# Optimization experiments

Hardware: AMD Instinct MI355X
Metric: run time of the kernel (lower is better)

The kernel has to match this reference:

```python
import jax, jax.numpy as jnp
import numpy as np

N, G, D, F, A = 50000, 128, 32, 64, 8
N_ITERS, N_BLAYERS = 3, 3
EPS = 1e-5
HIN = D + F + 2 * F * A  # 1120: input to transform_out


def setup_inputs() -> dict:
    key = jax.random.key(0)
    ks = jax.random.split(key, 10)
    p = lambda k, shape: jax.random.normal(k, shape, jnp.float32) * 0.05
    return {
        "x": jax.random.normal(ks[0], (N, 3), jnp.float32),
        "batch": jnp.sort(jax.random.randint(ks[1], (N,), 0, G)),
        # input_network: Linear(3,D) + LayerNorm(D) + Tanh
        "Wi": p(ks[2], (3, D)), "bi": jnp.zeros((D,), jnp.float32),
        "lni_w": jnp.ones((D,), jnp.float32), "lni_b": jnp.zeros((D,), jnp.float32),
        # 3 BipartiteLayers (weights shared across graph iterations, stacked over layer idx)
        "W_in": p(ks[3], (N_BLAYERS, D, F)), "b_in": jnp.zeros((N_BLAYERS, F), jnp.float32),
        "W_sc": p(ks[4], (N_BLAYERS, F, A)), "b_sc": jnp.zeros((N_BLAYERS, A), jnp.float32),
        "W_out": p(ks[5], (N_BLAYERS, HIN, D)), "b_out": jnp.zeros((N_BLAYERS, D), jnp.float32),
        # PyG graph-mode LayerNorm after each BipartiteLayer
        "gln_w": jnp.ones((N_BLAYERS, D), jnp.float32), "gln_b": jnp.zeros((N_BLAYERS, D), jnp.float32),
        "Wp": p(ks[6], (3, D, D)), "bp": jnp.zeros((3, D), jnp.float32),
        "lnp_w": jnp.ones((3, D), jnp.float32), "lnp_b": jnp.zeros((3, D), jnp.float32),
        "Wpo": p(ks[7], (D, 1)), "bpo": jnp.zeros((1,), jnp.float32),
    }


def _ln(x, w, b):  # nn.LayerNorm over last dim
    m = x.mean(-1, keepdims=True)
    v = ((x - m) ** 2).mean(-1, keepdims=True)
    return (x - m) / jnp.sqrt(v + EPS) * w + b


def _graph_ln(x, w, b):  # PyG gnn.norm.LayerNorm, mode='graph', batch=None
    xc = x - x.mean()
    std = jnp.sqrt((xc * xc).mean())
    return xc / (std + EPS) * w + b


def _bipartite(x, batch, counts, Win, bin_, Wsc, bsc, Wout, bout):
    xp = x @ Win + bin_                                  # (N,F)
    attn = jnp.exp(-jnp.abs(xp @ Wsc + bsc))             # (N,A) 'potential' activation
    w = attn[:, :, None] * xp[:, None, :]                # (N,A,F) == einsum('nf,na->naf')
    sums = jax.ops.segment_sum(w, batch, num_segments=G)  # (G,A,F)
    cnt = counts[:, None, None]
    mean_p = sums / jnp.maximum(cnt, 1.0)
    max_p = jax.ops.segment_max(w, batch, num_segments=G)
    max_p = jnp.where(cnt > 0, max_p, 0.0)               # torch_scatter zero-fill for empty
    agg = jnp.concatenate([mean_p, max_p], axis=-1).reshape(G, 2 * F * A)  # (G,A,2F)->(G,2FA)
    H = jnp.concatenate([x, xp, agg[batch]], axis=-1)    # (N, HIN)
    return jnp.tanh(H @ Wout + bout)                     # Tanh hidden activation


def reference(x, batch, Wi, bi, lni_w, lni_b, W_in, b_in, W_sc, b_sc, W_out, b_out,
              gln_w, gln_b, Wp, bp, lnp_w, lnp_b, Wpo, bpo):
    counts = jax.ops.segment_sum(jnp.ones((x.shape[0],), x.dtype), batch, num_segments=G)
    h = jnp.tanh(_ln(x @ Wi + bi, lni_w, lni_b))
    for _ in range(N_ITERS):
        for j in range(N_BLAYERS):
            h = _bipartite(h, batch, counts, W_in[j], b_in[j], W_sc[j], b_sc[j], W_out[j], b_out[j])
            h = _graph_ln(h, gln_w[j], gln_b[j])
    s = jax.ops.segment_sum(h, batch, num_segments=G) / jnp.maximum(counts, 1.0)[:, None]  # scatter_mean
    for j in range(3):
        s = jnp.tanh(_ln(s @ Wp[j] + bp[j], lnp_w[j], lnp_b[j]))
    return (s @ Wpo + bpo).squeeze(-1)  # (G,)
```

## Files before the change

kernel.cpp:

```cpp
#include <hip/hip_runtime.h>
#include <math.h>

#define NPTS 50000
#define NG   128
#define DD   32
#define FF   64
#define AA   8
#define HINC 1120
#define EPSV 1e-5f
#define CH   64

__device__ __forceinline__ float tanh_fast(float x) {
    float e = __expf(-2.f * fabsf(x));
    float r = __fdividef(1.f - e, 1.f + e);
    return copysignf(r, x);
}

__global__ __launch_bounds__(256) void k_setup(const int* __restrict__ batch,
                                               const float* __restrict__ W_in,
                                               const float* __restrict__ b_in,
                                               const float* __restrict__ W_out,
                                               const float* __restrict__ b_out,
                                               int* __restrict__ offs,
                                               float* __restrict__ stats,
                                               float* __restrict__ Weff,
                                               float* __restrict__ beff) {
    int t = threadIdx.x, bid = blockIdx.x;
    if (bid == 0) {
        if (t <= NG) {
            int lo = 0, hi = NPTS;
            while (lo < hi) { int mid = (lo+hi)>>1; if (batch[mid] < t) lo = mid+1; else hi = mid; }
            offs[t] = lo;
        }
        if (t < 32) stats[t] = 0.f;
    } else {
        int j = bid - 1;
        const float* W0 = W_out + (size_t)j*HINC*DD;
        const float* W1 = W0 + DD*DD;
        const float* Wi = W_in + (size_t)j*DD*FF;
        for (int e = t; e < DD*DD; e += 256) {
            int i = e >> 5, d = e & 31;
            float s = W0[e];
            for (int f = 0; f < FF; f++) s += Wi[i*FF+f] * W1[f*DD+d];
            Weff[j*DD*DD + e] = s;
        }
        if (t < DD) {
            float s = b_out[j*DD + t];
            for (int f = 0; f < FF; f++) s += b_in[j*FF+f] * W1[f*DD+t];
            beff[j*DD + t] = s;
        }
    }
}

__global__ __launch_bounds__(512) void k_L(const float* __restrict__ x,
                                           const float* __restrict__ Wi,
                                           const float* __restrict__ bi,
                                           const float* __restrict__ lniw,
                                           const float* __restrict__ lnib,
                                           const float* __restrict__ inb,
                                           const float* __restrict__ stats,
                                           const float* __restrict__ gw,
                                           const float* __restrict__ gb,
                                           const float* __restrict__ Win,
                                           const float* __restrict__ bin,
                                           const float* __restrict__ Wsc,
                                           const float* __restrict__ bsc,
                                           const int* __restrict__ offs,
                                           const float* __restrict__ Wagg,
                                           const float* __restrict__ beff,
                                           const float* __restrict__ Weff,
                                           float* __restrict__ tbuf,
                                           float* __restrict__ statsO,
                                           int isL0) {
    int g = blockIdx.x;
    int gs = offs[g], cnt = offs[g+1] - gs;
    const int t = threadIdx.x;
    if (cnt <= 0) return;

    __shared__ float hs[CH][36];
    __shared__ float sxp[CH][68];
    __shared__ float sattn[CH][9];
    __shared__ float sWin[DD*FF];
    __shared__ float sScT[AA*FF];
    __shared__ float sW[DD][36];
    __shared__ float agg[2*FF*AA];
    __shared__ float red[16][DD];
    __shared__ float aggWs[DD];
    __shared__ float sbin[FF];
    __shared__ float shW[DD];
    __shared__ float rs1[8], rs2[8];

    ((float4*)sWin)[t] = ((const float4*)Win)[t];
    { int a = t >> 6, f = t & 63; sScT[t] = Wsc[f*AA + a]; }
    for (int k = t; k < DD*DD; k += 512) sW[k >> 5][k & 31] = Weff[k];

    float gm = 0.f, ginv = 1.f;
    if (!isL0) {
        const float invM = 1.f/((float)NPTS*DD);
        gm = stats[0]*invM;
        float var = stats[1]*invM - gm*gm;
        ginv = 1.f/(sqrtf(fmaxf(var, 0.f)) + EPSV);
    }
    __syncthreads();
    if (!isL0) {
        if (t < FF) {
            float b = bin[t];
            for (int k = 0; k < DD; k++) {
                float sk = ginv * gw[k];
                float sh = gb[k] - gm * sk;
                b += sh * sWin[k*FF + t];
            }
            sbin[t] = b;
        } else if (t < FF + DD) {
            int d = t - FF;
            float r = 0.f;
            for (int k = 0; k < DD; k++) {
                float sk = ginv * gw[k];
                float sh = gb[k] - gm * sk;
                r += sh * sW[k][d];
            }
            shW[d] = r;
        }
        __syncthreads();
        for (int e = t; e < DD*FF; e += 512) sWin[e] *= ginv * gw[e >> 6];
        for (int e = t; e < DD*DD; e += 512) sW[e >> 5][e & 31] *= ginv * gw[e >> 5];
        __syncthreads();
    } else {
        if (t < FF) sbin[t] = bin[t];
        else if (t < FF + DD) shW[t - FF] = 0.f;
        __syncthreads();
    }

    const int pt = t >> 3, q = t & 7;
    const int fo = q * 8;
    const int ca = t >> 6, cf = t & 63;
    const float bscv = bsc[q];
    const float4 bi0 = *(const float4*)&sbin[fo];
    const float4 bi1 = *(const float4*)&sbin[fo+4];
    float csum = 0.f, cmax = -INFINITY;

    if (isL0) {
        for (int base = gs; base < gs + cnt; base += CH) {
            int np = min(CH, gs + cnt - base);
            __syncthreads();
            {
                int pp = t >> 3, d4 = (t & 7)*4;
                if (pp < np) {
                    int n = base + pp;
                    float x0 = x[n*3], x1 = x[n*3+1], x2 = x[n*3+2];
                    float tv0 = x0*Wi[d4+0] + x1*Wi[DD+d4+0] + x2*Wi[2*DD+d4+0] + bi[d4+0];
                    float tv1 = x0*Wi[d4+1] + x1*Wi[DD+d4+1] + x2*Wi[2*DD+d4+1] + bi[d4+1];
                    float tv2 = x0*Wi[d4+2] + x1*Wi[DD+d4+2] + x2*Wi[2*DD+d4+2] + bi[d4+2];
                    float tv3 = x0*Wi[d4+3] + x1*Wi[DD+d4+3] + x2*Wi[2*DD+d4+3] + bi[d4+3];
                    float sm = (tv0+tv1) + (tv2+tv3);
                    sm += __shfl_xor(sm, 1); sm += __shfl_xor(sm, 2); sm += __shfl_xor(sm, 4);
                    float mm = sm * (1.f/DD);
                    float c0 = tv0-mm, c1 = tv1-mm, c2 = tv2-mm, c3 = tv3-mm;
                    float qq = (c0*c0 + c1*c1) + (c2*c2 + c3*c3);
                    qq += __shfl_xor(qq, 1); qq += __shfl_xor(qq, 2); qq += __shfl_xor(qq, 4);
                    float inv = 1.f/sqrtf(qq*(1.f/DD) + EPSV);
                    hs[pp][d4+0] = tanh_fast(c0*inv*lniw[d4+0] + lnib[d4+0]);
                    hs[pp][d4+1] = tanh_fast(c1*inv*lniw[d4+1] + lnib[d4+1]);
                    hs[pp][d4+2] = tanh_fast(c2*inv*lniw[d4+2] + lnib[d4+2]);
                    hs[pp][d4+3] = tanh_fast(c3*inv*lniw[d4+3] + lnib[d4+3]);
                }
            }
            __syncthreads();
            if (pt < np) {
                float xr[8] = {bi0.x,bi0.y,bi0.z,bi0.w,bi1.x,bi1.y,bi1.z,bi1.w};
                #pragma unroll
                for (int k = 0; k < DD; k++) {
                    float hv = hs[pt][k];
                    float4 wa = *(const float4*)&sWin[k*FF + fo];
                    float4 wb = *(const float4*)&sWin[k*FF + fo + 4];
                    xr[0] += hv*wa.x; xr[1] += hv*wa.y; xr[2] += hv*wa.z; xr[3] += hv*wa.w;
                    xr[4] += hv*wb.x; xr[5] += hv*wb.y; xr[6] += hv*wb.z; xr[7] += hv*wb.w;
                }
                float pa[8];
                #pragma unroll
                for (int a = 0; a < 8; a++) {
                    float4 wa = *(const float4*)&sScT[a*FF + fo];
                    float4 wb = *(const float4*)&sScT[a*FF + fo + 4];
                    pa[a] = xr[0]*wa.x + xr[1]*wa.y + xr[2]*wa.z + xr[3]*wa.w
                          + xr[4]*wb.x + xr[5]*wb.y + xr[6]*wb.z + xr[7]*wb.w;
                }
                #pragma unroll
                for (int msk = 1; msk < 8; msk <<= 1) {
                    #pragma unroll
                    for (int a = 0; a < 8; a++) pa[a] += __shfl_xor(pa[a], msk);
                }
                sattn[pt][q] = __expf(-fabsf(pa[q] + bscv));
                *(float4*)&sxp[pt][fo]   = make_float4(xr[0],xr[1],xr[2],xr[3]);
                *(float4*)&sxp[pt][fo+4] = make_float4(xr[4],xr[5],xr[6],xr[7]);
            }
            __syncthreads();
            for (int pp = 0; pp < np; pp++) {
                float w = sattn[pp][ca] * sxp[pp][cf];
                csum += w; cmax = fmaxf(cmax, w);
            }
        }
    } else {
        float4 cur[8], nxt[8];
        {
            int n0 = gs + min(pt, cnt-1);
            const float4* r4 = (const float4*)(inb + (size_t)n0*DD);
            #pragma unroll
            for (int j = 0; j < 8; j++) cur[j] = r4[j];
        }
        for (int base = gs; base < gs + cnt; base += CH) {
            int np = min(CH, gs + cnt - base);
            {
                int nb = base + CH;
                int nclamp = (nb < gs + cnt) ? min(nb + pt, gs + cnt - 1) : gs;
                const float4* r4 = (const float4*)(inb + (size_t)nclamp*DD);
                #pragma unroll
                for (int j = 0; j < 8; j++) nxt[j] = r4[j];
            }
            __syncthreads();
            if (pt < np) {
                float xr[8] = {bi0.x,bi0.y,bi0.z,bi0.w,bi1.x,bi1.y,bi1.z,bi1.w};
                #pragma unroll
                for (int k4 = 0; k4 < 8; k4++) {
                    float hv0 = cur[k4].x, hv1 = cur[k4].y, hv2 = cur[k4].z, hv3 = cur[k4].w;
                    int kb = k4*4;
                    float4 wa, wb;
                    wa = *(const float4*)&sWin[(kb+0)*FF + fo]; wb = *(const float4*)&sWin[(kb+0)*FF + fo + 4];
                    xr[0]+=hv0*wa.x; xr[1]+=hv0*wa.y; xr[2]+=hv0*wa.z; xr[3]+=hv0*wa.w;
                    xr[4]+=hv0*wb.x; xr[5]+=hv0*wb.y; xr[6]+=hv0*wb.z; xr[7]+=hv0*wb.w;
                    wa = *(const float4*)&sWin[(kb+1)*FF + fo]; wb = *(const float4*)&sWin[(kb+1)*FF + fo + 4];
                    xr[0]+=hv1*wa.x; xr[1]+=hv1*wa.y; xr[2]+=hv1*wa.z; xr[3]+=hv1*wa.w;
                    xr[4]+=hv1*wb.x; xr[5]+=hv1*wb.y; xr[6]+=hv1*wb.z; xr[7]+=hv1*wb.w;
                    wa = *(const float4*)&sWin[(kb+2)*FF + fo]; wb = *(const float4*)&sWin[(kb+2)*FF + fo + 4];
                    xr[0]+=hv2*wa.x; xr[1]+=hv2*wa.y; xr[2]+=hv2*wa.z; xr[3]+=hv2*wa.w;
                    xr[4]+=hv2*wb.x; xr[5]+=hv2*wb.y; xr[6]+=hv2*wb.z; xr[7]+=hv2*wb.w;
                    wa = *(const float4*)&sWin[(kb+3)*FF + fo]; wb = *(const float4*)&sWin[(kb+3)*FF + fo + 4];
                    xr[0]+=hv3*wa.x; xr[1]+=hv3*wa.y; xr[2]+=hv3*wa.z; xr[3]+=hv3*wa.w;
                    xr[4]+=hv3*wb.x; xr[5]+=hv3*wb.y; xr[6]+=hv3*wb.z; xr[7]+=hv3*wb.w;
                }
                float pa[8];
                #pragma unroll
                for (int a = 0; a < 8; a++) {
                    float4 wa = *(const float4*)&sScT[a*FF + fo];
                    float4 wb = *(const float4*)&sScT[a*FF + fo + 4];
                    pa[a] = xr[0]*wa.x + xr[1]*wa.y + xr[2]*wa.z + xr[3]*wa.w
                          + xr[4]*wb.x + xr[5]*wb.y + xr[6]*wb.z + xr[7]*wb.w;
                }
                #pragma unroll
                for (int msk = 1; msk < 8; msk <<= 1) {
                    #pragma unroll
                    for (int a = 0; a < 8; a++) pa[a] += __shfl_xor(pa[a], msk);
                }
                sattn[pt][q] = __expf(-fabsf(pa[q] + bscv));
                *(float4*)&sxp[pt][fo]   = make_float4(xr[0],xr[1],xr[2],xr[3]);
                *(float4*)&sxp[pt][fo+4] = make_float4(xr[4],xr[5],xr[6],xr[7]);
            }
            __syncthreads();
            for (int pp = 0; pp < np; pp++) {
                float w = sattn[pp][ca] * sxp[pp][cf];
                csum += w; cmax = fmaxf(cmax, w);
            }
            #pragma unroll
            for (int j = 0; j < 8; j++) cur[j] = nxt[j];
        }
    }

    agg[ca*2*FF + cf]      = csum / (float)cnt;
    agg[ca*2*FF + FF + cf] = cmax;
    __syncthreads();
    {
        int d = t & 31, grp = t >> 5;
        float acc = 0.f;
        #pragma unroll
        for (int k2 = 0; k2 < 64; k2++) {
            int k = grp*64 + k2;
            acc += agg[k] * Wagg[k*DD + d];
        }
        red[grp][d] = acc;
    }
    __syncthreads();
    if (t < DD) {
        float r = 0.f;
        #pragma unroll
        for (int qq = 0; qq < 16; qq++) r += red[qq][t];
        aggWs[t] = r + beff[t] + shW[t];
    }
    __syncthreads();

    float s1 = 0.f, s2a = 0.f;
    const int d4 = q * 4;
    if (isL0) {
        for (int base = gs; base < gs + cnt; base += CH) {
            int np = min(CH, gs + cnt - base);
            __syncthreads();
            {
                int pp = t >> 3;
                if (pp < np) {
                    int n = base + pp;
                    float x0 = x[n*3], x1 = x[n*3+1], x2 = x[n*3+2];
                    float tv0 = x0*Wi[d4+0] + x1*Wi[DD+d4+0] + x2*Wi[2*DD+d4+0] + bi[d4+0];
                    float tv1 = x0*Wi[d4+1] + x1*Wi[DD+d4+1] + x2*Wi[2*DD+d4+1] + bi[d4+1];
                    float tv2 = x0*Wi[d4+2] + x1*Wi[DD+d4+2] + x2*Wi[2*DD+d4+2] + bi[d4+2];
                    float tv3 = x0*Wi[d4+3] + x1*Wi[DD+d4+3] + x2*Wi[2*DD+d4+3] + bi[d4+3];
                    float sm = (tv0+tv1) + (tv2+tv3);
                    sm += __shfl_xor(sm, 1); sm += __shfl_xor(sm, 2); sm += __shfl_xor(sm, 4);
                    float mm = sm * (1.f/DD);
                    float c0 = tv0-mm, c1 = tv1-mm, c2 = tv2-mm, c3 = tv3-mm;
                    float qq = (c0*c0 + c1*c1) + (c2*c2 + c3*c3);
                    qq += __shfl_xor(qq, 1); qq += __shfl_xor(qq, 2); qq += __shfl_xor(qq, 4);
                    float inv = 1.f/sqrtf(qq*(1.f/DD) + EPSV);
                    hs[pp][d4+0] = tanh_fast(c0*inv*lniw[d4+0] + lnib[d4+0]);
                    hs[pp][d4+1] = tanh_fast(c1*inv*lniw[d4+1] + lnib[d4+1]);
                    hs[pp][d4+2] = tanh_fast(c2*inv*lniw[d4+2] + lnib[d4+2]);
                    hs[pp][d4+3] = tanh_fast(c3*inv*lniw[d4+3] + lnib[d4+3]);
                }
            }
            __syncthreads();
            {
                int pp = t >> 3;
                if (pp < np) {
                    int n = base + pp;
                    float4 a0 = *(const float4*)&aggWs[d4];
                    float acc0 = a0.x, acc1 = a0.y, acc2 = a0.z, acc3 = a0.w;
                    #pragma unroll
                    for (int k = 0; k < DD; k++) {
                        float hv = hs[pp][k];
                        float4 w = *(const float4*)&sW[k][d4];
                        acc0 += hv*w.x; acc1 += hv*w.y; acc2 += hv*w.z; acc3 += hv*w.w;
                    }
                    float4 o;
                    o.x = tanh_fast(acc0); o.y = tanh_fast(acc1);
                    o.z = tanh_fast(acc2); o.w = tanh_fast(acc3);
                    *(float4*)&tbuf[(size_t)n*DD + d4] = o;
                    s1  += (o.x + o.y) + (o.z + o.w);
                    s2a += (o.x*o.x + o.y*o.y) + (o.z*o.z + o.w*o.w);
                }
            }
        }
    } else {
        float4 rcur[8], rnxt[8];
        if (pt < cnt) {
            {
                const float4* r4 = (const float4*)(inb + (size_t)(gs + pt)*DD);
                #pragma unroll
                for (int j = 0; j < 8; j++) rcur[j] = r4[j];
            }
            float4 a0 = *(const float4*)&aggWs[d4];
            for (int n = gs + pt; n < gs + cnt; n += CH) {
                int nn = n + CH;
                int nclamp = (nn < gs + cnt) ? nn : n;
                {
                    const float4* r4 = (const float4*)(inb + (size_t)nclamp*DD);
                    #pragma unroll
                    for (int j = 0; j < 8; j++) rnxt[j] = r4[j];
                }
                float acc0 = a0.x, acc1 = a0.y, acc2 = a0.z, acc3 = a0.w;
                #pragma unroll
                for (int k4 = 0; k4 < 8; k4++) {
                    float hv0 = rcur[k4].x, hv1 = rcur[k4].y, hv2 = rcur[k4].z, hv3 = rcur[k4].w;
                    int kb = k4*4;
                    float4 w;
                    w = *(const float4*)&sW[kb+0][d4];
                    acc0 += hv0*w.x; acc1 += hv0*w.y; acc2 += hv0*w.z; acc3 += hv0*w.w;
                    w = *(const float4*)&sW[kb+1][d4];
                    acc0 += hv1*w.x; acc1 += hv1*w.y; acc2 += hv1*w.z; acc3 += hv1*w.w;
                    w = *(const float4*)&sW[kb+2][d4];
                    acc0 += hv2*w.x; acc1 += hv2*w.y; acc2 += hv2*w.z; acc3 += hv2*w.w;
                    w = *(const float4*)&sW[kb+3][d4];
                    acc0 += hv3*w.x; acc1 += hv3*w.y; acc2 += hv3*w.z; acc3 += hv3*w.w;
                }
                float4 o;
                o.x = tanh_fast(acc0); o.y = tanh_fast(acc1);
                o.z = tanh_fast(acc2); o.w = tanh_fast(acc3);
                *(float4*)&tbuf[(size_t)n*DD + d4] = o;
                s1  += (o.x + o.y) + (o.z + o.w);
                s2a += (o.x*o.x + o.y*o.y) + (o.z*o.z + o.w*o.w);
                #pragma unroll
                for (int j = 0; j < 8; j++) rcur[j] = rnxt[j];
            }
        }
    }
    #pragma unroll
    for (int o = 32; o > 0; o >>= 1) { s1 += __shfl_down(s1, o); s2a += __shfl_down(s2a, o); }
    int wid = t >> 6;
    __syncthreads();
    if ((t & 63) == 0) { rs1[wid] = s1; rs2[wid] = s2a; }
    __syncthreads();
    if (t == 0) {
        float a1 = 0.f, a2 = 0.f;
        #pragma unroll
        for (int qq = 0; qq < 8; qq++) { a1 += rs1[qq]; a2 += rs2[qq]; }
        atomicAdd(&statsO[0], a1);
        atomicAdd(&statsO[1], a2);
    }
}

__global__ __launch_bounds__(256) void k_read(const float* __restrict__ tbuf,
                                              const float* __restrict__ stats,
                                              const float* __restrict__ gw,
                                              const float* __restrict__ gb,
                                              const int* __restrict__ offs,
                                              const float* __restrict__ Wp,
                                              const float* __restrict__ bp,
                                              const float* __restrict__ lnw,
                                              const float* __restrict__ lnb,
                                              const float* __restrict__ Wpo,
                                              const float* __restrict__ bpo,
                                              float* __restrict__ out) {
    int g = blockIdx.x;
    int t = threadIdx.x;
    int d = t & 31, pl = t >> 5;
    int s0 = offs[g], e0 = offs[g+1];
    float acc = 0.f;
    for (int n = s0 + pl; n < e0; n += 8) acc += tbuf[(size_t)n*DD + d];
    __shared__ float red[8][DD];
    red[pl][d] = acc;
    __syncthreads();
    __shared__ float sv[DD];
    if (t < DD) {
        float r = 0.f;
        #pragma unroll
        for (int qq = 0; qq < 8; qq++) r += red[qq][t];
        const float invM = 1.f/((float)NPTS*DD);
        float m = stats[0]*invM;
        float var = stats[1]*invM - m*m;
        float inv = 1.f/(sqrtf(fmaxf(var, 0.f)) + EPSV);
        float cnt = (float)(e0 - s0);
        float mean = r / fmaxf(cnt, 1.f);
        sv[t] = (e0 > s0) ? (mean - m)*inv*gw[t] + gb[t] : 0.f;
    }
    __syncthreads();
    for (int j = 0; j < 3; j++) {
        float yv = 0.f;
        if (t < DD) {
            float y = bp[j*DD + t];
            #pragma unroll
            for (int i = 0; i < DD; i++) y += sv[i] * Wp[j*DD*DD + i*DD + t];
            float sum = y;
            #pragma unroll
            for (int o = 1; o < 32; o <<= 1) sum += __shfl_xor(sum, o);
            float m = sum * (1.f/DD);
            float c = y - m;
            float sq = c*c;
            #pragma unroll
            for (int o = 1; o < 32; o <<= 1) sq += __shfl_xor(sq, o);
            float var = sq * (1.f/DD);
            yv = tanh_fast(c / sqrtf(var + EPSV) * lnw[j*DD+t] + lnb[j*DD+t]);
        }
        __syncthreads();
        if (t < DD) sv[t] = yv;
        __syncthreads();
    }
    if (t < DD) {
        float p = sv[t] * Wpo[t];
        #pragma unroll
        for (int o = 1; o < 32; o <<= 1) p += __shfl_xor(p, o);
        if (t == 0) out[g] = p + bpo[0];
    }
}

extern "C" void kernel_launch(void* const* d_in, const int* in_sizes, int n_in,
                              void* d_out, int out_size, void* d_ws, size_t ws_size,
                              hipStream_t stream) {
    const float* x     = (const float*)d_in[0];
    const int*   batch = (const int*)  d_in[1];
    const float* Wi    = (const float*)d_in[2];
    const float* bi    = (const float*)d_in[3];
    const float* lni_w = (const float*)d_in[4];
    const float* lni_b = (const float*)d_in[5];
    const float* W_in  = (const float*)d_in[6];
    const float* b_in  = (const float*)d_in[7];
    const float* W_sc  = (const float*)d_in[8];
    const float* b_sc  = (const float*)d_in[9];
    const float* W_out = (const float*)d_in[10];
    const float* b_out = (const float*)d_in[11];
    const float* gln_w = (const float*)d_in[12];
    const float* gln_b = (const float*)d_in[13];
    const float* Wp    = (const float*)d_in[14];
    const float* bp    = (const float*)d_in[15];
    const float* lnp_w = (const float*)d_in[16];
    const float* lnp_b = (const float*)d_in[17];
    const float* Wpo   = (const float*)d_in[18];
    const float* bpo   = (const float*)d_in[19];
    float* out = (float*)d_out;

    float* ws    = (float*)d_ws;
    float* tbuf  = ws;
    float* stats = tbuf + (size_t)NPTS*DD;
    float* Weff  = stats + 32;
    float* beff  = Weff + 3*DD*DD;
    int*   offs  = (int*)(beff + 3*DD);

    k_setup<<<4, 256, 0, stream>>>(batch, W_in, b_in, W_out, b_out, offs, stats, Weff, beff);

    for (int L = 0; L < 9; ++L) {
        int j = L % 3;
        int pj = (L + 2) % 3;
        const float* st  = L ? stats + 2*(L-1) : nullptr;
        const float* pgw = L ? gln_w + pj*DD : nullptr;
        const float* pgb = L ? gln_b + pj*DD : nullptr;
        k_L<<<NG, 512, 0, stream>>>(
            x, Wi, bi, lni_w, lni_b,
            tbuf, st, pgw, pgb,
            W_in + (size_t)j*DD*FF, b_in + j*FF,
            W_sc + (size_t)j*FF*AA, b_sc + j*AA,
            offs,
            W_out + (size_t)j*HINC*DD + (size_t)96*DD, beff + j*DD,
            Weff + (size_t)j*DD*DD, tbuf, stats + 2*L, (L == 0) ? 1 : 0);
    }
    k_read<<<NG, 256, 0, stream>>>(tbuf, stats + 16, gln_w + 2*DD, gln_b + 2*DD,
                                   offs, Wp, bp, lnp_w, lnp_b, Wpo, bpo, out);
}
```

Measured before the change: 352.5 us.

## Double block size to 1024 threads and split segment aggregation across halves

The per-graph kernel now launches 1024 threads, processes 128 points per chunk, and splits the mean/max aggregation into two halves that are merged through shared memory. The layer-0 input LayerNorm path now builds each point's hidden row in registers with wavefront shuffles instead of staging it through a shared-memory tile. This removes one barrier and one shared round trip per chunk. The aim is more parallelism per graph, since only 128 blocks run, at the cost of register pressure from the 1024-thread launch bound and an extra reduction step.

```diff
diff --git a/kernel.cpp b/kernel.cpp
--- a/kernel.cpp
+++ b/kernel.cpp
@@ -8,7 +8,8 @@
 #define AA   8
 #define HINC 1120
 #define EPSV 1e-5f
-#define CH   64
+#define CH   128
+#define NT   1024
 
 __device__ __forceinline__ float tanh_fast(float x) {
     float e = __expf(-2.f * fabsf(x));
@@ -52,32 +53,31 @@
     }
 }
 
-__global__ __launch_bounds__(512) void k_L(const float* __restrict__ x,
-                                           const float* __restrict__ Wi,
-                                           const float* __restrict__ bi,
-                                           const float* __restrict__ lniw,
-                                           const float* __restrict__ lnib,
-                                           const float* __restrict__ inb,
-                                           const float* __restrict__ stats,
-                                           const float* __restrict__ gw,
-                                           const float* __restrict__ gb,
-                                           const float* __restrict__ Win,
-                                           const float* __restrict__ bin,
-                                           const float* __restrict__ Wsc,
-                                           const float* __restrict__ bsc,
-                                           const int* __restrict__ offs,
-                                           const float* __restrict__ Wagg,
-                                           const float* __restrict__ beff,
-                                           const float* __restrict__ Weff,
-                                           float* __restrict__ tbuf,
-                                           float* __restrict__ statsO,
-                                           int isL0) {
+__global__ __launch_bounds__(NT, 1) void k_L(const float* __restrict__ x,
+                                             const float* __restrict__ Wi,
+                                             const float* __restrict__ bi,
+                                             const float* __restrict__ lniw,
+                                             const float* __restrict__ lnib,
+                                             const float* __restrict__ inb,
+                                             const float* __restrict__ stats,
+                                             const float* __restrict__ gw,
+                                             const float* __restrict__ gb,
+                                             const float* __restrict__ Win,
+                                             const float* __restrict__ bin,
+                                             const float* __restrict__ Wsc,
+                                             const float* __restrict__ bsc,
+                                             const int* __restrict__ offs,
+                                             const float* __restrict__ Wagg,
+                                             const float* __restrict__ beff,
+                                             const float* __restrict__ Weff,
+                                             float* __restrict__ tbuf,
+                                             float* __restrict__ statsO,
+                                             int isL0) {
     int g = blockIdx.x;
     int gs = offs[g], cnt = offs[g+1] - gs;
     const int t = threadIdx.x;
     if (cnt <= 0) return;
 
-    __shared__ float hs[CH][36];
     __shared__ float sxp[CH][68];
     __shared__ float sattn[CH][9];
     __shared__ float sWin[DD*FF];
@@ -88,11 +88,13 @@
     __shared__ float aggWs[DD];
     __shared__ float sbin[FF];
     __shared__ float shW[DD];
-    __shared__ float rs1[8], rs2[8];
-
-    ((float4*)sWin)[t] = ((const float4*)Win)[t];
-    { int a = t >> 6, f = t & 63; sScT[t] = Wsc[f*AA + a]; }
-    for (int k = t; k < DD*DD; k += 512) sW[k >> 5][k & 31] = Weff[k];
+    __shared__ float rs1[16], rs2[16];
+
+    if (t < 512) {
+        ((float4*)sWin)[t] = ((const float4*)Win)[t];
+        int a = t >> 6, f = t & 63; sScT[t] = Wsc[f*AA + a];
+    }
+    for (int k = t; k < DD*DD; k += NT) sW[k >> 5][k & 31] = Weff[k];
 
     float gm = 0.f, ginv = 1.f;
     if (!isL0) {
@@ -122,8 +124,8 @@
             shW[d] = r;
         }
         __syncthreads();
-        for (int e = t; e < DD*FF; e += 512) sWin[e] *= ginv * gw[e >> 6];
-        for (int e = t; e < DD*DD; e += 512) sW[e >> 5][e & 31] *= ginv * gw[e >> 5];
+        for (int e = t; e < DD*FF; e += NT) sWin[e] *= ginv * gw[e >> 6];
+        for (int e = t; e < DD*DD; e += NT) sW[e >> 5][e & 31] *= ginv * gw[e >> 5];
         __syncthreads();
     } else {
         if (t < FF) sbin[t] = bin[t];
@@ -132,142 +134,119 @@
     }
 
     const int pt = t >> 3, q = t & 7;
-    const int fo = q * 8;
-    const int ca = t >> 6, cf = t & 63;
+    const int fo = q * 8, d4 = q * 4;
+    const int c = t & 511, half = t >> 9;
+    const int ca = c >> 6, cf = c & 63;
     const float bscv = bsc[q];
     const float4 bi0 = *(const float4*)&sbin[fo];
     const float4 bi1 = *(const float4*)&sbin[fo+4];
     float csum = 0.f, cmax = -INFINITY;
 
-    if (isL0) {
-        for (int base = gs; base < gs + cnt; base += CH) {
-            int np = min(CH, gs + cnt - base);
-            __syncthreads();
-            {
-                int pp = t >> 3, d4 = (t & 7)*4;
-                if (pp < np) {
-                    int n = base + pp;
-                    float x0 = x[n*3], x1 = x[n*3+1], x2 = x[n*3+2];
-                    float tv0 = x0*Wi[d4+0] + x1*Wi[DD+d4+0] + x2*Wi[2*DD+d4+0] + bi[d4+0];
-                    float tv1 = x0*Wi[d4+1] + x1*Wi[DD+d4+1] + x2*Wi[2*DD+d4+1] + bi[d4+1];
-                    float tv2 = x0*Wi[d4+2] + x1*Wi[DD+d4+2] + x2*Wi[2*DD+d4+2] + bi[d4+2];
-                    float tv3 = x0*Wi[d4+3] + x1*Wi[DD+d4+3] + x2*Wi[2*DD+d4+3] + bi[d4+3];
-                    float sm = (tv0+tv1) + (tv2+tv3);
-                    sm += __shfl_xor(sm, 1); sm += __shfl_xor(sm, 2); sm += __shfl_xor(sm, 4);
-                    float mm = sm * (1.f/DD);
-                    float c0 = tv0-mm, c1 = tv1-mm, c2 = tv2-mm, c3 = tv3-mm;
-                    float qq = (c0*c0 + c1*c1) + (c2*c2 + c3*c3);
-                    qq += __shfl_xor(qq, 1); qq += __shfl_xor(qq, 2); qq += __shfl_xor(qq, 4);
-                    float inv = 1.f/sqrtf(qq*(1.f/DD) + EPSV);
-                    hs[pp][d4+0] = tanh_fast(c0*inv*lniw[d4+0] + lnib[d4+0]);
-                    hs[pp][d4+1] = tanh_fast(c1*inv*lniw[d4+1] + lnib[d4+1]);
-                    hs[pp][d4+2] = tanh_fast(c2*inv*lniw[d4+2] + lnib[d4+2]);
-                    hs[pp][d4+3] = tanh_fast(c3*inv*lniw[d4+3] + lnib[d4+3]);
-                }
-            }
-            __syncthreads();
-            if (pt < np) {
-                float xr[8] = {bi0.x,bi0.y,bi0.z,bi0.w,bi1.x,bi1.y,bi1.z,bi1.w};
-                #pragma unroll
-                for (int k = 0; k < DD; k++) {
-                    float hv = hs[pt][k];
-                    float4 wa = *(const float4*)&sWin[k*FF + fo];
-                    float4 wb = *(const float4*)&sWin[k*FF + fo + 4];
-                    xr[0] += hv*wa.x; xr[1] += hv*wa.y; xr[2] += hv*wa.z; xr[3] += hv*wa.w;
-                    xr[4] += hv*wb.x; xr[5] += hv*wb.y; xr[6] += hv*wb.z; xr[7] += hv*wb.w;
-                }
-                float pa[8];
-                #pragma unroll
-                for (int a = 0; a < 8; a++) {
-                    float4 wa = *(const float4*)&sScT[a*FF + fo];
-                    float4 wb = *(const float4*)&sScT[a*FF + fo + 4];
-                    pa[a] = xr[0]*wa.x + xr[1]*wa.y + xr[2]*wa.z + xr[3]*wa.w
-                          + xr[4]*wb.x + xr[5]*wb.y + xr[6]*wb.z + xr[7]*wb.w;
-                }
-                #pragma unroll
-                for (int msk = 1; msk < 8; msk <<= 1) {
-                    #pragma unroll
-                    for (int a = 0; a < 8; a++) pa[a] += __shfl_xor(pa[a], msk);
-                }
-                sattn[pt][q] = __expf(-fabsf(pa[q] + bscv));
-                *(float4*)&sxp[pt][fo]   = make_float4(xr[0],xr[1],xr[2],xr[3]);
-                *(float4*)&sxp[pt][fo+4] = make_float4(xr[4],xr[5],xr[6],xr[7]);
-            }
-            __syncthreads();
-            for (int pp = 0; pp < np; pp++) {
-                float w = sattn[pp][ca] * sxp[pp][cf];
-                csum += w; cmax = fmaxf(cmax, w);
-            }
-        }
-    } else {
-        float4 cur[8], nxt[8];
-        {
-            int n0 = gs + min(pt, cnt-1);
-            const float4* r4 = (const float4*)(inb + (size_t)n0*DD);
-            #pragma unroll
-            for (int j = 0; j < 8; j++) cur[j] = r4[j];
-        }
-        for (int base = gs; base < gs + cnt; base += CH) {
-            int np = min(CH, gs + cnt - base);
-            {
-                int nb = base + CH;
-                int nclamp = (nb < gs + cnt) ? min(nb + pt, gs + cnt - 1) : gs;
-                const float4* r4 = (const float4*)(inb + (size_t)nclamp*DD);
-                #pragma unroll
-                for (int j = 0; j < 8; j++) nxt[j] = r4[j];
-            }
-            __syncthreads();
-            if (pt < np) {
-                float xr[8] = {bi0.x,bi0.y,bi0.z,bi0.w,bi1.x,bi1.y,bi1.z,bi1.w};
-                #pragma unroll
-                for (int k4 = 0; k4 < 8; k4++) {
-                    float hv0 = cur[k4].x, hv1 = cur[k4].y, hv2 = cur[k4].z, hv3 = cur[k4].w;
-                    int kb = k4*4;
-                    float4 wa, wb;
-                    wa = *(const float4*)&sWin[(kb+0)*FF + fo]; wb = *(const float4*)&sWin[(kb+0)*FF + fo + 4];
-                    xr[0]+=hv0*wa.x; xr[1]+=hv0*wa.y; xr[2]+=hv0*wa.z; xr[3]+=hv0*wa.w;
-                    xr[4]+=hv0*wb.x; xr[5]+=hv0*wb.y; xr[6]+=hv0*wb.z; xr[7]+=hv0*wb.w;
-                    wa = *(const float4*)&sWin[(kb+1)*FF + fo]; wb = *(const float4*)&sWin[(kb+1)*FF + fo + 4];
-                    xr[0]+=hv1*wa.x; xr[1]+=hv1*wa.y; xr[2]+=hv1*wa.z; xr[3]+=hv1*wa.w;
-                    xr[4]+=hv1*wb.x; xr[5]+=hv1*wb.y; xr[6]+=hv1*wb.z; xr[7]+=hv1*wb.w;
-                    wa = *(const float4*)&sWin[(kb+2)*FF + fo]; wb = *(const float4*)&sWin[(kb+2)*FF + fo + 4];
-                    xr[0]+=hv2*wa.x; xr[1]+=hv2*wa.y; xr[2]+=hv2*wa.z; xr[3]+=hv2*wa.w;
-                    xr[4]+=hv2*wb.x; xr[5]+=hv2*wb.y; xr[6]+=hv2*wb.z; xr[7]+=hv2*wb.w;
-                    wa = *(const float4*)&sWin[(kb+3)*FF + fo]; wb = *(const float4*)&sWin[(kb+3)*FF + fo + 4];
-                    xr[0]+=hv3*wa.x; xr[1]+=hv3*wa.y; xr[2]+=hv3*wa.z; xr[3]+=hv3*wa.w;
-                    xr[4]+=hv3*wb.x; xr[5]+=hv3*wb.y; xr[6]+=hv3*wb.z; xr[7]+=hv3*wb.w;
-                }
-                float pa[8];
-                #pragma unroll
-                for (int a = 0; a < 8; a++) {
-                    float4 wa = *(const float4*)&sScT[a*FF + fo];
-                    float4 wb = *(const float4*)&sScT[a*FF + fo + 4];
-                    pa[a] = xr[0]*wa.x + xr[1]*wa.y + xr[2]*wa.z + xr[3]*wa.w
-                          + xr[4]*wb.x + xr[5]*wb.y + xr[6]*wb.z + xr[7]*wb.w;
-                }
-                #pragma unroll
-                for (int msk = 1; msk < 8; msk <<= 1) {
-                    #pragma unroll
-                    for (int a = 0; a < 8; a++) pa[a] += __shfl_xor(pa[a], msk);
-                }
-                sattn[pt][q] = __expf(-fabsf(pa[q] + bscv));
-                *(float4*)&sxp[pt][fo]   = make_float4(xr[0],xr[1],xr[2],xr[3]);
-                *(float4*)&sxp[pt][fo+4] = make_float4(xr[4],xr[5],xr[6],xr[7]);
-            }
-            __syncthreads();
-            for (int pp = 0; pp < np; pp++) {
-                float w = sattn[pp][ca] * sxp[pp][cf];
-                csum += w; cmax = fmaxf(cmax, w);
-            }
+    float4 cur[8], nxt[8];
+    if (!isL0) {
+        int n0 = gs + min(pt, cnt-1);
+        const float4* r4 = (const float4*)(inb + (size_t)n0*DD);
+        #pragma unroll
+        for (int j = 0; j < 8; j++) cur[j] = r4[j];
+    }
+    for (int base = gs; base < gs + cnt; base += CH) {
+        int np = min(CH, gs + cnt - base);
+        if (!isL0) {
+            int nb = base + CH;
+            int nclamp = (nb < gs + cnt) ? min(nb + pt, gs + cnt - 1) : gs;
+            const float4* r4 = (const float4*)(inb + (size_t)nclamp*DD);
+            #pragma unroll
+            for (int j = 0; j < 8; j++) nxt[j] = r4[j];
+        } else {
+            int n = base + min(pt, np-1);
+            float x0 = x[n*3], x1 = x[n*3+1], x2 = x[n*3+2];
+            float tv0 = x0*Wi[d4+0] + x1*Wi[DD+d4+0] + x2*Wi[2*DD+d4+0] + bi[d4+0];
+            float tv1 = x0*Wi[d4+1] + x1*Wi[DD+d4+1] + x2*Wi[2*DD+d4+1] + bi[d4+1];
+            float tv2 = x0*Wi[d4+2] + x1*Wi[DD+d4+2] + x2*Wi[2*DD+d4+2] + bi[d4+2];
+            float tv3 = x0*Wi[d4+3] + x1*Wi[DD+d4+3] + x2*Wi[2*DD+d4+3] + bi[d4+3];
+            float sm = (tv0+tv1) + (tv2+tv3);
+            sm += __shfl_xor(sm, 1); sm += __shfl_xor(sm, 2); sm += __shfl_xor(sm, 4);
+            float mm = sm * (1.f/DD);
+            float c0 = tv0-mm, c1 = tv1-mm, c2 = tv2-mm, c3 = tv3-mm;
+            float qq = (c0*c0 + c1*c1) + (c2*c2 + c3*c3);
+            qq += __shfl_xor(qq, 1); qq += __shfl_xor(qq, 2); qq += __shfl_xor(qq, 4);
+            float inv = 1.f/sqrtf(qq*(1.f/DD) + EPSV);
+            float o0 = tanh_fast(c0*inv*lniw[d4+0] + lnib[d4+0]);
+            float o1 = tanh_fast(c1*inv*lniw[d4+1] + lnib[d4+1]);
+            float o2 = tanh_fast(c2*inv*lniw[d4+2] + lnib[d4+2]);
+            float o3 = tanh_fast(c3*inv*lniw[d4+3] + lnib[d4+3]);
+            #pragma unroll
+            for (int j = 0; j < 8; j++) {
+                int src = (t & 56) | j;
+                cur[j].x = __shfl(o0, src, 64);
+                cur[j].y = __shfl(o1, src, 64);
+                cur[j].z = __shfl(o2, src, 64);
+                cur[j].w = __shfl(o3, src, 64);
+            }
+        }
+        __syncthreads();
+        if (pt < np) {
+            float xr[8] = {bi0.x,bi0.y,bi0.z,bi0.w,bi1.x,bi1.y,bi1.z,bi1.w};
+            #pragma unroll
+            for (int k4 = 0; k4 < 8; k4++) {
+                float hv0 = cur[k4].x, hv1 = cur[k4].y, hv2 = cur[k4].z, hv3 = cur[k4].w;
+                int kb = k4*4;
+                float4 wa, wb;
+                wa = *(const float4*)&sWin[(kb+0)*FF + fo]; wb = *(const float4*)&sWin[(kb+0)*FF + fo + 4];
+                xr[0]+=hv0*wa.x; xr[1]+=hv0*wa.y; xr[2]+=hv0*wa.z; xr[3]+=hv0*wa.w;
+                xr[4]+=hv0*wb.x; xr[5]+=hv0*wb.y; xr[6]+=hv0*wb.z; xr[7]+=hv0*wb.w;
+                wa = *(const float4*)&sWin[(kb+1)*FF + fo]; wb = *(const float4*)&sWin[(kb+1)*FF + fo + 4];
+                xr[0]+=hv1*wa.x; xr[1]+=hv1*wa.y; xr[2]+=hv1*wa.z; xr[3]+=hv1*wa.w;
+                xr[4]+=hv1*wb.x; xr[5]+=hv1*wb.y; xr[6]+=hv1*wb.z; xr[7]+=hv1*wb.w;
+                wa = *(const float4*)&sWin[(kb+2)*FF + fo]; wb = *(const float4*)&sWin[(kb+2)*FF + fo + 4];
+                xr[0]+=hv2*wa.x; xr[1]+=hv2*wa.y; xr[2]+=hv2*wa.z; xr[3]+=hv2*wa.w;
+                xr[4]+=hv2*wb.x; xr[5]+=hv2*wb.y; xr[6]+=hv2*wb.z; xr[7]+=hv2*wb.w;
+                wa = *(const float4*)&sWin[(kb+3)*FF + fo]; wb = *(const float4*)&sWin[(kb+3)*FF + fo + 4];
+                xr[0]+=hv3*wa.x; xr[1]+=hv3*wa.y; xr[2]+=hv3*wa.z; xr[3]+=hv3*wa.w;
+                xr[4]+=hv3*wb.x; xr[5]+=hv3*wb.y; xr[6]+=hv3*wb.z; xr[7]+=hv3*wb.w;
+            }
+            float pa[8];
+            #pragma unroll
+            for (int a = 0; a < 8; a++) {
+                float4 wa = *(const float4*)&sScT[a*FF + fo];
+                float4 wb = *(const float4*)&sScT[a*FF + fo + 4];
+                pa[a] = xr[0]*wa.x + xr[1]*wa.y + xr[2]*wa.z + xr[3]*wa.w
+                      + xr[4]*wb.x + xr[5]*wb.y + xr[6]*wb.z + xr[7]*wb.w;
+            }
+            #pragma unroll
+            for (int msk = 1; msk < 8; msk <<= 1) {
+                #pragma unroll
+                for (int a = 0; a < 8; a++) pa[a] += __shfl_xor(pa[a], msk);
+            }
+            sattn[pt][q] = __expf(-fabsf(pa[q] + bscv));
+            *(float4*)&sxp[pt][fo]   = make_float4(xr[0],xr[1],xr[2],xr[3]);
+            *(float4*)&sxp[pt][fo+4] = make_float4(xr[4],xr[5],xr[6],xr[7]);
+        }
+        __syncthreads();
+        int lo3 = half ? 64 : 0;
+        int hi3 = half ? np : min(np, 64);
+        for (int pp = lo3; pp < hi3; pp++) {
+            float w = sattn[pp][ca] * sxp[pp][cf];
+            csum += w; cmax = fmaxf(cmax, w);
+        }
+        if (!isL0) {
             #pragma unroll
             for (int j = 0; j < 8; j++) cur[j] = nxt[j];
         }
     }
 
-    agg[ca*2*FF + cf]      = csum / (float)cnt;
-    agg[ca*2*FF + FF + cf] = cmax;
-    __syncthreads();
-    {
+    __syncthreads();
+    if (t >= 512) { agg[c] = csum; ((float*)red)[c] = cmax; }
+    __syncthreads();
+    float fsum = csum, fmx = cmax;
+    if (t < 512) { fsum += agg[c]; fmx = fmaxf(fmx, ((float*)red)[c]); }
+    __syncthreads();
+    if (t < 512) {
+        agg[ca*2*FF + cf]      = fsum / (float)cnt;
+        agg[ca*2*FF + FF + cf] = fmx;
+    }
+    __syncthreads();
+    if (t < 512) {
         int d = t & 31, grp = t >> 5;
         float acc = 0.f;
         #pragma unroll
@@ -287,64 +266,64 @@
     __syncthreads();
 
     float s1 = 0.f, s2a = 0.f;
-    const int d4 = q * 4;
-    if (isL0) {
-        for (int base = gs; base < gs + cnt; base += CH) {
-            int np = min(CH, gs + cnt - base);
-            __syncthreads();
-            {
-                int pp = t >> 3;
-                if (pp < np) {
-                    int n = base + pp;
-                    float x0 = x[n*3], x1 = x[n*3+1], x2 = x[n*3+2];
-                    float tv0 = x0*Wi[d4+0] + x1*Wi[DD+d4+0] + x2*Wi[2*DD+d4+0] + bi[d4+0];
-                    float tv1 = x0*Wi[d4+1] + x1*Wi[DD+d4+1] + x2*Wi[2*DD+d4+1] + bi[d4+1];
-                    float tv2 = x0*Wi[d4+2] + x1*Wi[DD+d4+2] + x2*Wi[2*DD+d4+2] + bi[d4+2];
-                    float tv3 = x0*Wi[d4+3] + x1*Wi[DD+d4+3] + x2*Wi[2*DD+d4+3] + bi[d4+3];
-                    float sm = (tv0+tv1) + (tv2+tv3);
-                    sm += __shfl_xor(sm, 1); sm += __shfl_xor(sm, 2); sm += __shfl_xor(sm, 4);
-                    float mm = sm * (1.f/DD);
-                    float c0 = tv0-mm, c1 = tv1-mm, c2 = tv2-mm, c3 = tv3-mm;
-                    float qq = (c0*c0 + c1*c1) + (c2*c2 + c3*c3);
-                    qq += __shfl_xor(qq, 1); qq += __shfl_xor(qq, 2); qq += __shfl_xor(qq, 4);
-                    float inv = 1.f/sqrtf(qq*(1.f/DD) + EPSV);
-                    hs[pp][d4+0] = tanh_fast(c0*inv*lniw[d4+0] + lnib[d4+0]);
-                    hs[pp][d4+1] = tanh_fast(c1*inv*lniw[d4+1] + lnib[d4+1]);
-                    hs[pp][d4+2] = tanh_fast(c2*inv*lniw[d4+2] + lnib[d4+2]);
-                    hs[pp][d4+3] = tanh_fast(c3*inv*lniw[d4+3] + lnib[d4+3]);
+    if (pt < cnt) {
+        float4 a0 = *(const float4*)&aggWs[d4];
+        if (isL0) {
+            for (int n = gs + pt; n < gs + cnt; n += CH) {
+                float x0 = x[n*3], x1 = x[n*3+1], x2 = x[n*3+2];
+                float tv0 = x0*Wi[d4+0] + x1*Wi[DD+d4+0] + x2*Wi[2*DD+d4+0] + bi[d4+0];
+                float tv1 = x0*Wi[d4+1] + x1*Wi[DD+d4+1] + x2*Wi[2*DD+d4+1] + bi[d4+1];
+                float tv2 = x0*Wi[d4+2] + x1*Wi[DD+d4+2] + x2*Wi[2*DD+d4+2] + bi[d4+2];
+                float tv3 = x0*Wi[d4+3] + x1*Wi[DD+d4+3] + x2*Wi[2*DD+d4+3] + bi[d4+3];
+                float sm = (tv0+tv1) + (tv2+tv3);
+                sm += __shfl_xor(sm, 1); sm += __shfl_xor(sm, 2); sm += __shfl_xor(sm, 4);
+                float mm = sm * (1.f/DD);
+                float c0 = tv0-mm, c1 = tv1-mm, c2 = tv2-mm, c3 = tv3-mm;
+                float qq = (c0*c0 + c1*c1) + (c2*c2 + c3*c3);
+                qq += __shfl_xor(qq, 1); qq += __shfl_xor(qq, 2); qq += __shfl_xor(qq, 4);
+                float inv = 1.f/sqrtf(qq*(1.f/DD) + EPSV);
+                float o0 = tanh_fast(c0*inv*lniw[d4+0] + lnib[d4+0]);
+                float o1 = tanh_fast(c1*inv*lniw[d4+1] + lnib[d4+1]);
+                float o2 = tanh_fast(c2*inv*lniw[d4+2] + lnib[d4+2]);
+                float o3 = tanh_fast(c3*inv*lniw[d4+3] + lnib[d4+3]);
+                float4 row[8];
+                #pragma unroll
+                for (int j = 0; j < 8; j++) {
+                    int src = (t & 56) | j;
+                    row[j].x = __shfl(o0, src, 64);
+                    row[j].y = __shfl(o1, src, 64);
+                    row[j].z = __shfl(o2, src, 64);
+                    row[j].w = __shfl(o3, src, 64);
                 }
-            }
-            __syncthreads();
-            {
-                int pp = t >> 3;
-                if (pp < np) {
-                    int n = base + pp;
-                    float4 a0 = *(const float4*)&aggWs[d4];
-                    float acc0 = a0.x, acc1 = a0.y, acc2 = a0.z, acc3 = a0.w;
-                    #pragma unroll
-                    for (int k = 0; k < DD; k++) {
-                        float hv = hs[pp][k];
-                        float4 w = *(const float4*)&sW[k][d4];
-                        acc0 += hv*w.x; acc1 += hv*w.y; acc2 += hv*w.z; acc3 += hv*w.w;
-                    }
-                    float4 o;
-                    o.x = tanh_fast(acc0); o.y = tanh_fast(acc1);
-                    o.z = tanh_fast(acc2); o.w = tanh_fast(acc3);
-                    *(float4*)&tbuf[(size_t)n*DD + d4] = o;
-                    s1  += (o.x + o.y) + (o.z + o.w);
-                    s2a += (o.x*o.x + o.y*o.y) + (o.z*o.z + o.w*o.w);
+                float acc0 = a0.x, acc1 = a0.y, acc2 = a0.z, acc3 = a0.w;
+                #pragma unroll
+                for (int k4 = 0; k4 < 8; k4++) {
+                    float hv0 = row[k4].x, hv1 = row[k4].y, hv2 = row[k4].z, hv3 = row[k4].w;
+                    int kb = k4*4;
+                    float4 w;
+                    w = *(const float4*)&sW[kb+0][d4];
+                    acc0 += hv0*w.x; acc1 += hv0*w.y; acc2 += hv0*w.z; acc3 += hv0*w.w;
+                    w = *(const float4*)&sW[kb+1][d4];
+                    acc0 += hv1*w.x; acc1 += hv1*w.y; acc2 += hv1*w.z; acc3 += hv1*w.w;
+                    w = *(const float4*)&sW[kb+2][d4];
+                    acc0 += hv2*w.x; acc1 += hv2*w.y; acc2 += hv2*w.z; acc3 += hv2*w.w;
+                    w = *(const float4*)&sW[kb+3][d4];
+                    acc0 += hv3*w.x; acc1 += hv3*w.y; acc2 += hv3*w.z; acc3 += hv3*w.w;
                 }
-            }
-        }
-    } else {
-        float4 rcur[8], rnxt[8];
-        if (pt < cnt) {
+                float4 o;
+                o.x = tanh_fast(acc0); o.y = tanh_fast(acc1);
+                o.z = tanh_fast(acc2); o.w = tanh_fast(acc3);
+                *(float4*)&tbuf[(size_t)n*DD + d4] = o;
+                s1  += (o.x + o.y) + (o.z + o.w);
+                s2a += (o.x*o.x + o.y*o.y) + (o.z*o.z + o.w*o.w);
+            }
+        } else {
+            float4 rcur[8], rnxt[8];
             {
                 const float4* r4 = (const float4*)(inb + (size_t)(gs + pt)*DD);
                 #pragma unroll
                 for (int j = 0; j < 8; j++) rcur[j] = r4[j];
             }
-            float4 a0 = *(const float4*)&aggWs[d4];
             for (int n = gs + pt; n < gs + cnt; n += CH) {
                 int nn = n + CH;
                 int nclamp = (nn < gs + cnt) ? nn : n;
@@ -388,7 +367,7 @@
     if (t == 0) {
         float a1 = 0.f, a2 = 0.f;
         #pragma unroll
-        for (int qq = 0; qq < 8; qq++) { a1 += rs1[qq]; a2 += rs2[qq]; }
+        for (int qq = 0; qq < 16; qq++) { a1 += rs1[qq]; a2 += rs2[qq]; }
         atomicAdd(&statsO[0], a1);
         atomicAdd(&statsO[1], a2);
     }
@@ -498,7 +477,7 @@
         const float* st  = L ? stats + 2*(L-1) : nullptr;
         const float* pgw = L ? gln_w + pj*DD : nullptr;
         const float* pgb = L ? gln_b + pj*DD : nullptr;
-        k_L<<<NG, 512, 0, stream>>>(
+        k_L<<<NG, NT, 0, stream>>>(
             x, Wi, bi, lni_w, lni_b,
             tbuf, st, pgw, pgb,
             W_in + (size_t)j*DD*FF, b_in + j*FF,
```

Result: slower. 895.1 us (+154.0%).
